# Kernel tuning notes

Hardware: AMD Instinct MI355X
Metric: run time of the kernel (lower is better)

## Reference

```python
import jax, jax.numpy as jnp
import numpy as np

H, DK, DV, S = 16, 1024, 1024, 2048
DH_QK = DK // H  # 64, per-head q/k dim
DH_V = DV // H   # 64, per-head v dim


def setup_inputs() -> dict:
    key = jax.random.key(0)
    ks = jax.random.split(key, 11)
    init = lambda k, shape, fan_in: jax.random.uniform(k, shape, jnp.float32, -1.0, 1.0) / jnp.sqrt(jnp.float32(fan_in))
    return {
        "Q": jax.random.normal(ks[0], (S, DK), jnp.float32),
        "K": jax.random.normal(ks[1], (S, DK), jnp.float32),
        "V": jax.random.normal(ks[2], (S, DV), jnp.float32),
        # per-head Linear weights, torch convention [out, in] stacked over heads
        "Wq": init(ks[3], (H, DH_QK, DH_QK), DH_QK),
        "bq": init(ks[4], (H, DH_QK), DH_QK),
        "Wk": init(ks[5], (H, DH_QK, DH_QK), DH_QK),
        "bk": init(ks[6], (H, DH_QK), DH_QK),
        "Wv": init(ks[7], (H, DH_V, DH_V), DH_V),
        "bv": init(ks[8], (H, DH_V), DH_V),
        "Wo": init(ks[9], (DK, H * DH_V), H * DH_V),  # final linear: d_model x (h*dv_h)
        "bo": init(ks[10], (DK,), H * DH_V),
    }


def reference(Q, K, V, Wq, bq, Wk, bk, Wv, bv, Wo, bo):
    h, dh = Wq.shape[0], Wq.shape[2]
    dv = Wv.shape[2]
    s = Q.shape[0]
    # split features into h per-head chunks (same as slicing loop in torch)
    Qh = Q.reshape(s, h, dh)
    Kh = K.reshape(s, h, dh)
    Vh = V.reshape(s, h, dv)
    # per-head Linear: x @ W.T + b, batched over heads
    q = jnp.einsum('shd,hed->she', Qh, Wq) + bq
    k = jnp.einsum('shd,hed->she', Kh, Wk) + bk
    v = jnp.einsum('shd,hed->she', Vh, Wv) + bv
    # scaled dot-product attention per head
    scores = jnp.einsum('she,the->hst', q, k) / jnp.sqrt(jnp.float32(dh))
    attn = jax.nn.softmax(scores, axis=-1)
    o = jnp.einsum('hst,the->she', attn, v)  # [s, h, dv]
    concat = o.reshape(s, h * dv)
    return concat @ Wo.T + bo
```

## Files before the change

kernel.cpp:

```cpp
#include <hip/hip_runtime.h>
#include <stdint.h>

static constexpr int H   = 16;
static constexpr int S   = 2048;
static constexpr int DHd = 64;
static constexpr int DM  = 1024;
static constexpr int NSPLIT = 4;
static constexpr int KT_PER_SPLIT = (S / 64) / NSPLIT;

using f32x4   = __attribute__((ext_vector_type(4))) float;
using f32x8   = __attribute__((ext_vector_type(8))) float;
using f32x16  = __attribute__((ext_vector_type(16))) float;
using short8  = __attribute__((ext_vector_type(8))) short;
using bf16x8  = __attribute__((ext_vector_type(8))) __bf16;
using uint4v  = __attribute__((ext_vector_type(4))) unsigned int;

#if __has_builtin(__builtin_amdgcn_exp2f)
#define EXP2F __builtin_amdgcn_exp2f
#else
#define EXP2F exp2f
#endif

__device__ __forceinline__ short f2bf(float f) {
  union { float f; uint32_t u; } v; v.f = f;
  uint32_t r = v.u + 0x7FFFu + ((v.u >> 16) & 1u);
  return (short)(r >> 16);
}
__device__ __forceinline__ float bf2f(short s) {
  union { uint32_t u; float f; } v;
  v.u = ((uint32_t)(unsigned short)s) << 16;
  return v.f;
}

__device__ __forceinline__ short8 f2bf8(f32x4 a, f32x4 b) {
  short8 v;
  v[0] = f2bf(a[0]); v[1] = f2bf(a[1]); v[2] = f2bf(a[2]); v[3] = f2bf(a[3]);
  v[4] = f2bf(b[0]); v[5] = f2bf(b[1]); v[6] = f2bf(b[2]); v[7] = f2bf(b[3]);
  return v;
}

__device__ __forceinline__ unsigned int pkbf(float a, float b) {
  __bf16 x = (__bf16)a, y = (__bf16)b;
  unsigned short ux = __builtin_bit_cast(unsigned short, x);
  unsigned short uy = __builtin_bit_cast(unsigned short, y);
  return (unsigned int)ux | ((unsigned int)uy << 16);
}

__device__ __forceinline__ f32x4 mfma16(short8 a, short8 b, f32x4 c) {
  return __builtin_amdgcn_mfma_f32_16x16x32_bf16(
      __builtin_bit_cast(bf16x8, a), __builtin_bit_cast(bf16x8, b), c, 0, 0, 0);
}
__device__ __forceinline__ f32x16 mfma32(short8 a, short8 b, f32x16 c) {
  return __builtin_amdgcn_mfma_f32_32x32x16_bf16(
      __builtin_bit_cast(bf16x8, a), __builtin_bit_cast(bf16x8, b), c, 0, 0, 0);
}

__device__ __forceinline__ short8 lds_read_swz(const short* base, int row, int chunk) {
  return *(const short8*)((const char*)base + row * 128 + ((chunk ^ (row & 7)) << 4));
}
__device__ __forceinline__ void lds_write_swz(short* base, int row, int chunk, short8 v) {
  *(short8*)((char*)base + row * 128 + ((chunk ^ (row & 7)) << 4)) = v;
}

using u32g = __attribute__((address_space(1))) const unsigned int;
using u32l = __attribute__((address_space(3))) unsigned int;
__device__ __forceinline__ void gl_lds16(const short* g, short* l) {
  __builtin_amdgcn_global_load_lds(
      reinterpret_cast<u32g*>(reinterpret_cast<uintptr_t>(g)),
      reinterpret_cast<u32l*>(static_cast<unsigned int>(reinterpret_cast<uintptr_t>(l))),
      16, 0, 0);
}

__global__ __launch_bounds__(256) void proj_kernel(
    const float* __restrict__ Q, const float* __restrict__ K, const float* __restrict__ V,
    const float* __restrict__ Wq, const float* __restrict__ bq,
    const float* __restrict__ Wk, const float* __restrict__ bk,
    const float* __restrict__ Wv, const float* __restrict__ bv,
    const float* __restrict__ Wo, short* __restrict__ wob,
    short* __restrict__ qb, short* __restrict__ kb, short* __restrict__ vtb) {
  const int t = threadIdx.x;
  const int mode = blockIdx.z;

  if (mode == 3) {
    int chunk = blockIdx.y * gridDim.x + blockIdx.x;
    int i = (chunk * 256 + t) * 16;
    f32x4 x0 = *(const f32x4*)(Wo + i);
    f32x4 x1 = *(const f32x4*)(Wo + i + 4);
    f32x4 x2 = *(const f32x4*)(Wo + i + 8);
    f32x4 x3 = *(const f32x4*)(Wo + i + 12);
    *(short8*)(wob + i)     = f2bf8(x0, x1);
    *(short8*)(wob + i + 8) = f2bf8(x2, x3);
    return;
  }

  const int h  = blockIdx.y;
  const int rt = blockIdx.x * 128;

  const float* X; const float* W; const float* bias;
  if (mode == 0)      { X = Q; W = Wq; bias = bq; }
  else if (mode == 1) { X = K; W = Wk; bias = bk; }
  else                { X = V; W = Wv; bias = bv; }
  bias += h * DHd;
  const float scale = (mode == 0) ? 0.125f * 1.44269504f : 1.0f;

  __shared__ short Xs[128 * 64];
  __shared__ short Ws[64 * 64];
  __shared__ short Ot[64 * 136];

#pragma unroll
  for (int p = 0; p < 4; p++) {
    int ci = p * 256 + t;
    int row = ci >> 3, oct = ci & 7;
    const float* g = X + (size_t)(rt + row) * DM + h * DHd + oct * 8;
    f32x4 x0 = *(const f32x4*)g;
    f32x4 x1 = *(const f32x4*)(g + 4);
    lds_write_swz(Xs, row, oct, f2bf8(x0, x1));
  }
#pragma unroll
  for (int p = 0; p < 2; p++) {
    int ci = p * 256 + t;
    int row = ci >> 3, oct = ci & 7;
    const float* g = W + (size_t)h * DHd * DHd + row * DHd + oct * 8;
    f32x4 x0 = *(const f32x4*)g;
    f32x4 x1 = *(const f32x4*)(g + 4);
    lds_write_swz(Ws, row, oct, f2bf8(x0, x1));
  }
  __syncthreads();

  const int wid = t >> 6, lane = t & 63;
  const int l15 = lane & 15, l4 = lane >> 4;

  f32x4 acc[2][4] = {};
#pragma unroll
  for (int ks = 0; ks < 2; ks++) {
    int chunk = ks * 4 + l4;
    short8 a0 = lds_read_swz(Xs, wid * 32 + l15, chunk);
    short8 a1 = lds_read_swz(Xs, wid * 32 + 16 + l15, chunk);
#pragma unroll
    for (int nf = 0; nf < 4; nf++) {
      short8 b = lds_read_swz(Ws, nf * 16 + l15, chunk);
      acc[0][nf] = mfma16(a0, b, acc[0][nf]);
      acc[1][nf] = mfma16(a1, b, acc[1][nf]);
    }
  }

  if (mode < 2) {
    short* out = (mode == 0) ? qb : kb;
#pragma unroll
    for (int mf = 0; mf < 2; mf++)
#pragma unroll
      for (int nf = 0; nf < 4; nf++) {
        int col = nf * 16 + l15;
        float b = bias[col];
#pragma unroll
        for (int r = 0; r < 4; r++) {
          int row = rt + wid * 32 + mf * 16 + l4 * 4 + r;
          out[((size_t)h * S + row) * DHd + col] = f2bf((acc[mf][nf][r] + b) * scale);
        }
      }
  } else {
#pragma unroll
    for (int mf = 0; mf < 2; mf++)
#pragma unroll
      for (int nf = 0; nf < 4; nf++) {
        int col = nf * 16 + l15;
        float b = bias[col];
#pragma unroll
        for (int r = 0; r < 4; r++) {
          int lrow = wid * 32 + mf * 16 + l4 * 4 + r;
          Ot[col * 136 + lrow] = f2bf(acc[mf][nf][r] + b);
        }
      }
    __syncthreads();
#pragma unroll
    for (int p = 0; p < 2; p++) {
      int ci = p * 256 + t;
      int e = ci >> 3, c16 = ci & 7;
      short8 a = *(const short8*)&Ot[e * 136 + c16 * 16];
      short8 b = *(const short8*)&Ot[e * 136 + c16 * 16 + 8];
      short8 lo, hi;
      lo[0] = a[0]; lo[1] = a[1]; lo[2] = a[2]; lo[3] = a[3];
      lo[4] = b[0]; lo[5] = b[1]; lo[6] = b[2]; lo[7] = b[3];
      hi[0] = a[4]; hi[1] = a[5]; hi[2] = a[6]; hi[3] = a[7];
      hi[4] = b[4]; hi[5] = b[5]; hi[6] = b[6]; hi[7] = b[7];
      short* dst = vtb + ((size_t)h * DHd + e) * S + rt + c16 * 16;
      *(short8*)dst       = lo;
      *(short8*)(dst + 8) = hi;
    }
  }
}

__global__ __launch_bounds__(256, 2) void attn_kernel(
    const short* __restrict__ qb, const short* __restrict__ kb,
    const short* __restrict__ vtb, short* __restrict__ OpT,
    float* __restrict__ lbuf) {
  const int h  = blockIdx.x;
  const int sp = blockIdx.y;
  const int t = threadIdx.x, wid = t >> 6, lane = t & 63;
  const int l31 = lane & 31, l5 = lane >> 5;
  const int qw = blockIdx.z * 256 + wid * 64;

  __shared__ short Ks[3][64 * 64];
  __shared__ short Vs[3][64 * 64];

  short8 qf[2][4];
#pragma unroll
  for (int tt = 0; tt < 2; tt++) {
    const short* qrow = qb + ((size_t)h * S + qw + tt * 32 + l31) * DHd;
#pragma unroll
    for (int c = 0; c < 4; c++) qf[tt][c] = *(const short8*)(qrow + c * 16 + l5 * 8);
  }

  const int srow8 = lane >> 3, schunk = lane & 7;
  const int r0 = wid * 16 + srow8, r1 = r0 + 8;
  const int kt0 = sp * KT_PER_SPLIT;
  const short* kg0 = kb + ((size_t)h * S + (size_t)kt0 * 64 + r0) * DHd + ((schunk ^ (r0 & 7)) * 8);
  const short* kg1 = kb + ((size_t)h * S + (size_t)kt0 * 64 + r1) * DHd + ((schunk ^ (r1 & 7)) * 8);
  const short* vg0 = vtb + ((size_t)h * DHd + r0) * S + (size_t)kt0 * 64 + ((schunk ^ (r0 & 7)) * 8);
  const short* vg1 = vtb + ((size_t)h * DHd + r1) * S + (size_t)kt0 * 64 + ((schunk ^ (r1 & 7)) * 8);

  auto stage = [&](int buf, int kk) {
    const size_t ka = (size_t)kk * 64 * DHd;
    const size_t va = (size_t)kk * 64;
    gl_lds16(kg0 + ka, &Ks[buf][wid * 1024]);
    gl_lds16(kg1 + ka, &Ks[buf][wid * 1024 + 512]);
    gl_lds16(vg0 + va, &Vs[buf][wid * 1024]);
    gl_lds16(vg1 + va, &Vs[buf][wid * 1024 + 512]);
  };

  stage(0, 0);
  stage(1, 1);

  f32x16 oa00 = {}, oa01 = {}, oa10 = {}, oa11 = {};
  f32x8 lac0 = {}, lac1 = {};

  for (int kk = 0; kk < KT_PER_SPLIT; kk++) {
    const int cur = kk % 3;
    if (kk + 1 < KT_PER_SPLIT) asm volatile("s_waitcnt vmcnt(4)" ::: "memory");
    else                       asm volatile("s_waitcnt vmcnt(0)" ::: "memory");
    __syncthreads();
    if (kk + 2 < KT_PER_SPLIT) stage((kk + 2) % 3, kk + 2);

    f32x16 s00 = {}, s01 = {}, s10 = {}, s11 = {};
    __builtin_amdgcn_s_setprio(1);
#pragma unroll
    for (int c = 0; c < 4; c++) {
      short8 ak0 = lds_read_swz(Ks[cur], l31, 2 * c + l5);
      short8 ak1 = lds_read_swz(Ks[cur], 32 + l31, 2 * c + l5);
      s00 = mfma32(ak0, qf[0][c], s00);
      s01 = mfma32(ak1, qf[0][c], s01);
      s10 = mfma32(ak0, qf[1][c], s10);
      s11 = mfma32(ak1, qf[1][c], s11);
    }
    __builtin_amdgcn_s_setprio(0);

#pragma unroll
    for (int i = 0; i < 16; i++) {
      float p00 = EXP2F(s00[i]), p01 = EXP2F(s01[i]);
      float p10 = EXP2F(s10[i]), p11 = EXP2F(s11[i]);
      s00[i] = p00; s01[i] = p01; s10[i] = p10; s11[i] = p11;
      lac0[i & 7] += p00 + p01;
      lac1[i & 7] += p10 + p11;
    }

    unsigned int pk0[2][8], pk1[2][8];
#pragma unroll
    for (int g = 0; g < 4; g++) {
      pk0[0][g * 2 + 0] = pkbf(s00[4 * g + 0], s00[4 * g + 1]);
      pk0[0][g * 2 + 1] = pkbf(s00[4 * g + 2], s00[4 * g + 3]);
      pk0[1][g * 2 + 0] = pkbf(s01[4 * g + 0], s01[4 * g + 1]);
      pk0[1][g * 2 + 1] = pkbf(s01[4 * g + 2], s01[4 * g + 3]);
      pk1[0][g * 2 + 0] = pkbf(s10[4 * g + 0], s10[4 * g + 1]);
      pk1[0][g * 2 + 1] = pkbf(s10[4 * g + 2], s10[4 * g + 3]);
      pk1[1][g * 2 + 0] = pkbf(s11[4 * g + 0], s11[4 * g + 1]);
      pk1[1][g * 2 + 1] = pkbf(s11[4 * g + 2], s11[4 * g + 3]);
    }

    __builtin_amdgcn_s_setprio(1);
#pragma unroll
    for (int j = 0; j < 4; j++) {
      const int bb = j >> 1;
      const int s4 = (j & 1) * 4;
      short8 av0 = lds_read_swz(Vs[cur], l31, 2 * j + l5);
      short8 av1 = lds_read_swz(Vs[cur], 32 + l31, 2 * j + l5);
      uint4v pf0, pf1;
      pf0[0] = pk0[bb][s4 + 0]; pf0[1] = pk0[bb][s4 + 1];
      pf0[2] = pk0[bb][s4 + 2]; pf0[3] = pk0[bb][s4 + 3];
      pf1[0] = pk1[bb][s4 + 0]; pf1[1] = pk1[bb][s4 + 1];
      pf1[2] = pk1[bb][s4 + 2]; pf1[3] = pk1[bb][s4 + 3];
      short8 p0 = __builtin_bit_cast(short8, pf0);
      short8 p1 = __builtin_bit_cast(short8, pf1);
      oa00 = mfma32(av0, p0, oa00);
      oa01 = mfma32(av1, p0, oa01);
      oa10 = mfma32(av0, p1, oa10);
      oa11 = mfma32(av1, p1, oa11);
    }
    __builtin_amdgcn_s_setprio(0);
  }

#pragma unroll
  for (int st = 4; st >= 1; st >>= 1)
#pragma unroll
    for (int i = 0; i < st; i++) { lac0[i] += lac0[i + st]; lac1[i] += lac1[i + st]; }
  float l0 = lac0[0] + __shfl_xor(lac0[0], 32);
  float l1 = lac1[0] + __shfl_xor(lac1[0], 32);

#pragma unroll
  for (int r = 0; r < 16; r++) {
    int dvb = (r & 3) + 8 * (r >> 2) + 4 * l5;
    size_t base = (((size_t)sp * H + h) * DHd + dvb) * S + qw + l31;
    OpT[base]            = f2bf(oa00[r]);
    OpT[base + 32UL * S] = f2bf(oa01[r]);
    OpT[base + 32]            = f2bf(oa10[r]);
    OpT[base + 32UL * S + 32] = f2bf(oa11[r]);
  }
  if (l5 == 0) {
    lbuf[((size_t)sp * H + h) * S + qw + l31]      = l0;
    lbuf[((size_t)sp * H + h) * S + qw + 32 + l31] = l1;
  }
}

__global__ __launch_bounds__(256) void combine_kernel(
    const short* __restrict__ OpT, const float* __restrict__ lbuf,
    short* __restrict__ Ob) {
  const int h  = blockIdx.y;
  const int s0 = blockIdx.x * 64;
  __shared__ short tile[64][72];

  const int t = threadIdx.x;
  const int sl = t & 63, dvg = t >> 6;
  const int s = s0 + sl;

  float lt = 0.f;
#pragma unroll
  for (int sp = 0; sp < NSPLIT; sp++)
    lt += lbuf[((size_t)sp * H + h) * S + s];
  float inv = 1.0f / lt;

  float val[16];
#pragma unroll
  for (int p = 0; p < 16; p++) {
    int dv = dvg * 16 + p;
    float o = 0.f;
#pragma unroll
    for (int sp = 0; sp < NSPLIT; sp++)
      o += bf2f(OpT[(((size_t)sp * H + h) * DHd + dv) * S + s]);
    val[p] = o * inv;
  }
  short8 v0, v1;
#pragma unroll
  for (int i = 0; i < 8; i++) { v0[i] = f2bf(val[i]); v1[i] = f2bf(val[8 + i]); }
  *(short8*)&tile[sl][dvg * 16]     = v0;
  *(short8*)&tile[sl][dvg * 16 + 8] = v1;
  __syncthreads();

#pragma unroll
  for (int i = 0; i < 2; i++) {
    int cid = t + i * 256;
    int r = cid >> 3, c = cid & 7;
    short8 v = *(const short8*)&tile[r][c * 8];
    *(short8*)(Ob + (size_t)(s0 + r) * DM + h * DHd + c * 8) = v;
  }
}

__global__ __launch_bounds__(256) void out_gemm(
    const short* __restrict__ Ob, const short* __restrict__ wob,
    const float* __restrict__ bo, float* __restrict__ out) {
  const int m0 = blockIdx.x * 64;
  const int n0 = blockIdx.y * 64;
  constexpr int KT = DM / 64;

  __shared__ short As[3][64 * 64];
  __shared__ short Bs[3][64 * 64];

  const int t = threadIdx.x, wid = t >> 6, lane = t & 63;
  const int l15 = lane & 15, l4 = lane >> 4;
  const int srow8 = lane >> 3, schunk = lane & 7;
  const int r0 = wid * 16 + srow8, r1 = r0 + 8;

  const short* ag0 = Ob  + (size_t)(m0 + r0) * DM + ((schunk ^ (r0 & 7)) * 8);
  const short* ag1 = Ob  + (size_t)(m0 + r1) * DM + ((schunk ^ (r1 & 7)) * 8);
  const short* bg0 = wob + (size_t)(n0 + r0) * DM + ((schunk ^ (r0 & 7)) * 8);
  const short* bg1 = wob + (size_t)(n0 + r1) * DM + ((schunk ^ (r1 & 7)) * 8);

  auto stage = [&](int buf, int kc) {
    const int off = kc * 64;
    gl_lds16(ag0 + off, &As[buf][wid * 1024]);
    gl_lds16(ag1 + off, &As[buf][wid * 1024 + 512]);
    gl_lds16(bg0 + off, &Bs[buf][wid * 1024]);
    gl_lds16(bg1 + off, &Bs[buf][wid * 1024 + 512]);
  };

  stage(0, 0);
  stage(1, 1);

  f32x4 acc[4] = {};
  for (int kc = 0; kc < KT; kc++) {
    const int cur = kc % 3;
    if (kc + 1 < KT) asm volatile("s_waitcnt vmcnt(4)" ::: "memory");
    else             asm volatile("s_waitcnt vmcnt(0)" ::: "memory");
    __syncthreads();
    if (kc + 2 < KT) stage((kc + 2) % 3, kc + 2);
#pragma unroll
    for (int ks = 0; ks < 2; ks++) {
      int chunk = ks * 4 + l4;
      short8 a = lds_read_swz(As[cur], wid * 16 + l15, chunk);
#pragma unroll
      for (int nf = 0; nf < 4; nf++) {
        short8 b = lds_read_swz(Bs[cur], nf * 16 + l15, chunk);
        acc[nf] = mfma16(a, b, acc[nf]);
      }
    }
  }
#pragma unroll
  for (int nf = 0; nf < 4; nf++) {
    int col = n0 + nf * 16 + l15;
    float b = bo[col];
#pragma unroll
    for (int r = 0; r < 4; r++) {
      int row = m0 + wid * 16 + l4 * 4 + r;
      out[(size_t)row * DM + col] = acc[nf][r] + b;
    }
  }
}

extern "C" void kernel_launch(void* const* d_in, const int* in_sizes, int n_in,
                              void* d_out, int out_size, void* d_ws, size_t ws_size,
                              hipStream_t stream) {
  const float* Q  = (const float*)d_in[0];
  const float* K  = (const float*)d_in[1];
  const float* V  = (const float*)d_in[2];
  const float* Wq = (const float*)d_in[3];
  const float* bq = (const float*)d_in[4];
  const float* Wk = (const float*)d_in[5];
  const float* bk = (const float*)d_in[6];
  const float* Wv = (const float*)d_in[7];
  const float* bv = (const float*)d_in[8];
  const float* Wo = (const float*)d_in[9];
  const float* bo = (const float*)d_in[10];

  char* ws = (char*)d_ws;
  short* qb   = (short*)(ws);
  short* kb   = (short*)(ws + ((size_t)4 << 20));
  short* vtb  = (short*)(ws + ((size_t)8 << 20));
  short* Obf  = (short*)(ws + ((size_t)12 << 20));
  short* wob  = (short*)(ws + ((size_t)16 << 20));
  short* OpT  = (short*)(ws + ((size_t)18 << 20));
  float* lbuf = (float*)(ws + ((size_t)34 << 20));

  proj_kernel<<<dim3(S / 128, H, 4), 256, 0, stream>>>(Q, K, V, Wq, bq, Wk, bk, Wv, bv,
                                                       Wo, wob, qb, kb, vtb);
  attn_kernel<<<dim3(H, NSPLIT, S / 256), 256, 0, stream>>>(qb, kb, vtb, OpT, lbuf);
  combine_kernel<<<dim3(S / 64, H), 256, 0, stream>>>(OpT, lbuf, Obf);
  out_gemm<<<dim3(S / 64, DM / 64), 256, 0, stream>>>(Obf, wob, bo, (float*)d_out);
}
```

Measured before the change: 52.01 us.

## Compute softmax row sums via MFMA with ones and use 32x32 MFMA in out GEMM

```diff
diff --git a/kernel.cpp b/kernel.cpp
--- a/kernel.cpp
+++ b/kernel.cpp
@@ -9,7 +9,6 @@
 static constexpr int KT_PER_SPLIT = (S / 64) / NSPLIT;
 
 using f32x4   = __attribute__((ext_vector_type(4))) float;
-using f32x8   = __attribute__((ext_vector_type(8))) float;
 using f32x16  = __attribute__((ext_vector_type(16))) float;
 using short8  = __attribute__((ext_vector_type(8))) short;
 using bf16x8  = __attribute__((ext_vector_type(8))) __bf16;
@@ -203,6 +202,10 @@
   __shared__ short Ks[3][64 * 64];
   __shared__ short Vs[3][64 * 64];
 
+  short8 ones;
+#pragma unroll
+  for (int i = 0; i < 8; i++) ones[i] = (short)0x3F80;
+
   short8 qf[2][4];
 #pragma unroll
   for (int tt = 0; tt < 2; tt++) {
@@ -232,7 +235,7 @@
   stage(1, 1);
 
   f32x16 oa00 = {}, oa01 = {}, oa10 = {}, oa11 = {};
-  f32x8 lac0 = {}, lac1 = {};
+  f32x16 lm0 = {}, lm1 = {};
 
   for (int kk = 0; kk < KT_PER_SPLIT; kk++) {
     const int cur = kk % 3;
@@ -256,11 +259,10 @@
 
 #pragma unroll
     for (int i = 0; i < 16; i++) {
-      float p00 = EXP2F(s00[i]), p01 = EXP2F(s01[i]);
-      float p10 = EXP2F(s10[i]), p11 = EXP2F(s11[i]);
-      s00[i] = p00; s01[i] = p01; s10[i] = p10; s11[i] = p11;
-      lac0[i & 7] += p00 + p01;
-      lac1[i & 7] += p10 + p11;
+      s00[i] = EXP2F(s00[i]);
+      s01[i] = EXP2F(s01[i]);
+      s10[i] = EXP2F(s10[i]);
+      s11[i] = EXP2F(s11[i]);
     }
 
     unsigned int pk0[2][8], pk1[2][8];
@@ -292,18 +294,16 @@
       short8 p1 = __builtin_bit_cast(short8, pf1);
       oa00 = mfma32(av0, p0, oa00);
       oa01 = mfma32(av1, p0, oa01);
+      lm0  = mfma32(ones, p0, lm0);
       oa10 = mfma32(av0, p1, oa10);
       oa11 = mfma32(av1, p1, oa11);
+      lm1  = mfma32(ones, p1, lm1);
     }
     __builtin_amdgcn_s_setprio(0);
   }
 
-#pragma unroll
-  for (int st = 4; st >= 1; st >>= 1)
-#pragma unroll
-    for (int i = 0; i < st; i++) { lac0[i] += lac0[i + st]; lac1[i] += lac1[i + st]; }
-  float l0 = lac0[0] + __shfl_xor(lac0[0], 32);
-  float l1 = lac1[0] + __shfl_xor(lac1[0], 32);
+  float l0 = lm0[0];
+  float l1 = lm1[0];
 
 #pragma unroll
   for (int r = 0; r < 16; r++) {
@@ -374,7 +374,8 @@
   __shared__ short Bs[3][64 * 64];
 
   const int t = threadIdx.x, wid = t >> 6, lane = t & 63;
-  const int l15 = lane & 15, l4 = lane >> 4;
+  const int l31 = lane & 31, l5 = lane >> 5;
+  const int wr = wid >> 1, wn = wid & 1;
   const int srow8 = lane >> 3, schunk = lane & 7;
   const int r0 = wid * 16 + srow8, r1 = r0 + 8;
 
@@ -394,7 +395,7 @@
   stage(0, 0);
   stage(1, 1);
 
-  f32x4 acc[4] = {};
+  f32x16 acc = {};
   for (int kc = 0; kc < KT; kc++) {
     const int cur = kc % 3;
     if (kc + 1 < KT) asm volatile("s_waitcnt vmcnt(4)" ::: "memory");
@@ -402,25 +403,18 @@
     __syncthreads();
     if (kc + 2 < KT) stage((kc + 2) % 3, kc + 2);
 #pragma unroll
-    for (int ks = 0; ks < 2; ks++) {
-      int chunk = ks * 4 + l4;
-      short8 a = lds_read_swz(As[cur], wid * 16 + l15, chunk);
-#pragma unroll
-      for (int nf = 0; nf < 4; nf++) {
-        short8 b = lds_read_swz(Bs[cur], nf * 16 + l15, chunk);
-        acc[nf] = mfma16(a, b, acc[nf]);
-      }
-    }
-  }
-#pragma unroll
-  for (int nf = 0; nf < 4; nf++) {
-    int col = n0 + nf * 16 + l15;
-    float b = bo[col];
-#pragma unroll
-    for (int r = 0; r < 4; r++) {
-      int row = m0 + wid * 16 + l4 * 4 + r;
-      out[(size_t)row * DM + col] = acc[nf][r] + b;
-    }
+    for (int c = 0; c < 4; c++) {
+      short8 a = lds_read_swz(As[cur], wr * 32 + l31, 2 * c + l5);
+      short8 b = lds_read_swz(Bs[cur], wn * 32 + l31, 2 * c + l5);
+      acc = mfma32(a, b, acc);
+    }
+  }
+  const int col = n0 + wn * 32 + l31;
+  const float bb = bo[col];
+#pragma unroll
+  for (int r = 0; r < 16; r++) {
+    int row = m0 + wr * 32 + (r & 3) + 8 * (r >> 2) + 4 * l5;
+    out[(size_t)row * DM + col] = acc[r] + bb;
   }
 }
 
```

After: 52.63 us. Within noise of the previous version (+1.2%).

## Coalesce q/k projection stores, vectorize combine loads, use 32x32 MFMA in out GEMM

Applied to the files above, without the earlier changes.

```diff
diff --git a/kernel.cpp b/kernel.cpp
--- a/kernel.cpp
+++ b/kernel.cpp
@@ -105,7 +105,7 @@
 
   __shared__ short Xs[128 * 64];
   __shared__ short Ws[64 * 64];
-  __shared__ short Ot[64 * 136];
+  __shared__ short Ot[128 * 72];
 
 #pragma unroll
   for (int p = 0; p < 4; p++) {
@@ -154,10 +154,18 @@
         float b = bias[col];
 #pragma unroll
         for (int r = 0; r < 4; r++) {
-          int row = rt + wid * 32 + mf * 16 + l4 * 4 + r;
-          out[((size_t)h * S + row) * DHd + col] = f2bf((acc[mf][nf][r] + b) * scale);
+          int lrow = wid * 32 + mf * 16 + l4 * 4 + r;
+          Ot[lrow * 72 + col] = f2bf((acc[mf][nf][r] + b) * scale);
         }
       }
+    __syncthreads();
+#pragma unroll
+    for (int p = 0; p < 4; p++) {
+      int ci = p * 256 + t;
+      int row = ci >> 3, c8 = ci & 7;
+      short8 v = *(const short8*)&Ot[row * 72 + c8 * 8];
+      *(short8*)(out + ((size_t)h * S + rt + row) * DHd + c8 * 8) = v;
+    }
   } else {
 #pragma unroll
     for (int mf = 0; mf < 2; mf++)
@@ -328,30 +336,37 @@
   __shared__ short tile[64][72];
 
   const int t = threadIdx.x;
-  const int sl = t & 63, dvg = t >> 6;
-  const int s = s0 + sl;
-
-  float lt = 0.f;
-#pragma unroll
-  for (int sp = 0; sp < NSPLIT; sp++)
-    lt += lbuf[((size_t)sp * H + h) * S + s];
-  float inv = 1.0f / lt;
-
-  float val[16];
-#pragma unroll
-  for (int p = 0; p < 16; p++) {
-    int dv = dvg * 16 + p;
-    float o = 0.f;
-#pragma unroll
-    for (int sp = 0; sp < NSPLIT; sp++)
-      o += bf2f(OpT[(((size_t)sp * H + h) * DHd + dv) * S + s]);
-    val[p] = o * inv;
-  }
-  short8 v0, v1;
-#pragma unroll
-  for (int i = 0; i < 8; i++) { v0[i] = f2bf(val[i]); v1[i] = f2bf(val[8 + i]); }
-  *(short8*)&tile[sl][dvg * 16]     = v0;
-  *(short8*)&tile[sl][dvg * 16 + 8] = v1;
+  const int dvh = t >> 3;
+  const int sb  = (t & 7) * 8;
+
+  float lt[8] = {};
+#pragma unroll
+  for (int sp = 0; sp < NSPLIT; sp++) {
+    const float* lp = lbuf + ((size_t)sp * H + h) * S + s0 + sb;
+    f32x4 a = *(const f32x4*)lp;
+    f32x4 b = *(const f32x4*)(lp + 4);
+#pragma unroll
+    for (int i = 0; i < 4; i++) { lt[i] += a[i]; lt[4 + i] += b[i]; }
+  }
+  float inv[8];
+#pragma unroll
+  for (int i = 0; i < 8; i++) inv[i] = 1.0f / lt[i];
+
+#pragma unroll
+  for (int half = 0; half < 2; half++) {
+    const int dv = dvh + half * 32;
+    float acc[8] = {};
+#pragma unroll
+    for (int sp = 0; sp < NSPLIT; sp++) {
+      const short* op = OpT + (((size_t)sp * H + h) * DHd + dv) * S + s0 + sb;
+      short8 v = *(const short8*)op;
+#pragma unroll
+      for (int i = 0; i < 8; i++) acc[i] += bf2f(v[i]);
+    }
+#pragma unroll
+    for (int i = 0; i < 8; i++)
+      tile[sb + i][dv] = f2bf(acc[i] * inv[i]);
+  }
   __syncthreads();
 
 #pragma unroll
@@ -374,7 +389,8 @@
   __shared__ short Bs[3][64 * 64];
 
   const int t = threadIdx.x, wid = t >> 6, lane = t & 63;
-  const int l15 = lane & 15, l4 = lane >> 4;
+  const int l31 = lane & 31, l5 = lane >> 5;
+  const int wr = wid >> 1, wn = wid & 1;
   const int srow8 = lane >> 3, schunk = lane & 7;
   const int r0 = wid * 16 + srow8, r1 = r0 + 8;
 
@@ -394,7 +410,7 @@
   stage(0, 0);
   stage(1, 1);
 
-  f32x4 acc[4] = {};
+  f32x16 acc = {};
   for (int kc = 0; kc < KT; kc++) {
     const int cur = kc % 3;
     if (kc + 1 < KT) asm volatile("s_waitcnt vmcnt(4)" ::: "memory");
@@ -402,25 +418,18 @@
     __syncthreads();
     if (kc + 2 < KT) stage((kc + 2) % 3, kc + 2);
 #pragma unroll
-    for (int ks = 0; ks < 2; ks++) {
-      int chunk = ks * 4 + l4;
-      short8 a = lds_read_swz(As[cur], wid * 16 + l15, chunk);
-#pragma unroll
-      for (int nf = 0; nf < 4; nf++) {
-        short8 b = lds_read_swz(Bs[cur], nf * 16 + l15, chunk);
-        acc[nf] = mfma16(a, b, acc[nf]);
-      }
-    }
-  }
-#pragma unroll
-  for (int nf = 0; nf < 4; nf++) {
-    int col = n0 + nf * 16 + l15;
-    float b = bo[col];
-#pragma unroll
-    for (int r = 0; r < 4; r++) {
-      int row = m0 + wid * 16 + l4 * 4 + r;
-      out[(size_t)row * DM + col] = acc[nf][r] + b;
-    }
+    for (int c = 0; c < 4; c++) {
+      short8 a = lds_read_swz(As[cur], wr * 32 + l31, 2 * c + l5);
+      short8 b = lds_read_swz(Bs[cur], wn * 32 + l31, 2 * c + l5);
+      acc = mfma32(a, b, acc);
+    }
+  }
+  const int col = n0 + wn * 32 + l31;
+  const float bb = bo[col];
+#pragma unroll
+  for (int r = 0; r < 16; r++) {
+    int row = m0 + wr * 32 + (r & 3) + 8 * (r >> 2) + 4 * l5;
+    out[(size_t)row * DM + col] = acc[r] + bb;
   }
 }
 
```

Result: no change. 52.42 us, median of 2 (+0.8%).
